# Kernel tuning notes

Measured on AMD Instinct MI355X. Metric: run time of the kernel, lower is better.

The kernel has to match this reference:

```python
import jax, jax.numpy as jnp
import numpy as np

STU_N, EXER_N, K_N, EMB = 20000, 20000, 128, 128
BATCH = 4096

def _pos(w):
    # PosLinear weight transform: 2*relu(-w) + w  (== |w|)
    return 2.0 * jax.nn.relu(-w) + w

def setup_inputs() -> dict:
    key = jax.random.key(0)
    ks = jax.random.split(key, 12)
    xav = lambda k, shape: jax.random.normal(k, shape, jnp.float32) * np.sqrt(2.0 / sum(shape))
    return {
        "stu_id": jax.random.randint(ks[0], (BATCH,), 0, STU_N, jnp.int32),
        "exer_id": jax.random.randint(ks[1], (BATCH,), 0, EXER_N, jnp.int32),
        "kq": jax.random.uniform(ks[2], (BATCH, K_N), jnp.float32),
        "student_q": xav(ks[3], (STU_N, EMB)),
        "exercise_k": xav(ks[4], (EXER_N, EMB)),
        "student_v": xav(ks[5], (STU_N, EMB)),
        "exercise_v": xav(ks[6], (EXER_N, EMB)),
        "knowledge_v": xav(ks[7], (K_N, EMB)),
        "W1": xav(ks[8], (EMB, 2 * EMB)), "b1": jnp.zeros((EMB,), jnp.float32),
        "W2": xav(ks[9], (EMB, 2 * EMB)), "b2": jnp.zeros((EMB,), jnp.float32),
        "W3": xav(ks[10], (1, EMB)), "b3": jnp.zeros((1,), jnp.float32),
    }

def reference(stu_id, exer_id, kq, student_q, exercise_k, student_v, exercise_v,
              knowledge_v, W1, b1, W2, b2, W3, b3):
    stu_q = student_q[stu_id]          # (B, D)
    exer_k = exercise_k[exer_id]       # (B, D)
    stu_v = student_v[stu_id]          # (B, D)
    exer_v = exercise_v[exer_id]       # (B, D)
    B, D = stu_v.shape
    K = knowledge_v.shape[0]

    kn = jnp.broadcast_to(knowledge_v[None, :, :], (B, K, D))
    stu_b = jnp.broadcast_to(stu_v[:, None, :], (B, K, D))
    exer_b = jnp.broadcast_to(exer_v[:, None, :], (B, K, D))

    # PosLinear 1/2 on concat([x, kn]) -> split GEMM avoids materializing concat
    W1p, W2p, W3p = _pos(W1), _pos(W2), _pos(W3)
    pref = jax.nn.sigmoid(jnp.einsum('bkd,ed->bke', jnp.concatenate([stu_b, kn], -1), W1p) + b1)
    diff = jax.nn.sigmoid(jnp.einsum('bkd,ed->bke', jnp.concatenate([exer_b, kn], -1), W2p) + b2)

    disc = jax.nn.sigmoid(stu_q * exer_k)              # (B, D)
    input_x = (pref - diff) * disc[:, None, :]         # (B, K, D)
    o = jax.nn.sigmoid(jnp.einsum('bkd,od->bko', input_x, W3p) + b3)  # (B, K, 1)

    sum_out = jnp.sum(o * kq[:, :, None], axis=1)      # (B, 1)
    count = jnp.sum(kq, axis=1, keepdims=True)         # (B, 1)
    return jnp.squeeze(sum_out / count)                # (B,)
```

## Files before the change

kernel.cpp:

```cpp
#include <hip/hip_runtime.h>

#define D  128
#define KN 128
#define NB 16
#define LOG2E 1.44269504088896340736f

__device__ __forceinline__ float negexp(float v) {
    return __builtin_amdgcn_exp2f(v * -LOG2E);
}
__device__ __forceinline__ float sigf(float x) {
    return __builtin_amdgcn_rcpf(1.0f + negexp(x));
}

__device__ __forceinline__ void emit_row(
    float4* __restrict__ P, int b, int eg,
    const float4& as, const float4& ae,
    const float* __restrict__ stu_q, const float* __restrict__ exer_k,
    const float* __restrict__ kq, const float* __restrict__ W3,
    int sid, int eid)
{
    float4 sq = *(const float4*)(stu_q + sid * D + eg * 4);
    float4 ek = *(const float4*)(exer_k + eid * D + eg * 4);
    float4 kv = *(const float4*)(kq + b * D + eg * 4);
    float4 w3 = *(const float4*)(W3 + eg * 4);
    float4* Pb = P + b * D + eg * 4;
    Pb[0] = make_float4(negexp(as.x), negexp(ae.x), sigf(sq.x * ek.x) * fabsf(w3.x), kv.x);
    Pb[1] = make_float4(negexp(as.y), negexp(ae.y), sigf(sq.y * ek.y) * fabsf(w3.y), kv.y);
    Pb[2] = make_float4(negexp(as.z), negexp(ae.z), sigf(sq.z * ek.z) * fabsf(w3.z), kv.z);
    Pb[3] = make_float4(negexp(as.w), negexp(ae.w), sigf(sq.w * ek.w) * fabsf(w3.w), kv.w);
}

__global__ __launch_bounds__(512) void k1_kernel(
    const int* __restrict__ stu_id, const int* __restrict__ exer_id,
    const float* __restrict__ kq,
    const float* __restrict__ stu_q, const float* __restrict__ exer_k,
    const float* __restrict__ stu_v, const float* __restrict__ exer_v,
    const float* __restrict__ kn,
    const float* __restrict__ W1, const float* __restrict__ b1,
    const float* __restrict__ W2, const float* __restrict__ b2,
    const float* __restrict__ W3,
    float4* __restrict__ P, float* __restrict__ TABGf, int B)
{
    __shared__ float W1T[D][132];
    __shared__ float W2T[D][132];
    __shared__ float SV[NB][D];
    __shared__ float EV[NB][D];
    __shared__ int sids[NB], eids[NB];

    const int tid = threadIdx.x;
    const int b0  = blockIdx.x * NB;

    if (tid < NB) {
        int b = b0 + tid;
        sids[tid] = stu_id[b < B ? b : 0];
        eids[tid] = exer_id[b < B ? b : 0];
    }
    for (int i = tid; i < D * D; i += 512) {
        int e = i >> 7, d = i & (D - 1);
        W1T[d][e] = fabsf(W1[e * (2 * D) + d]);
        W2T[d][e] = fabsf(W2[e * (2 * D) + d]);
    }
    __syncthreads();
    for (int i = tid; i < NB * D; i += 512) {
        int bi = i >> 7, d = i & (D - 1);
        SV[bi][d] = stu_v[sids[bi] * D + d];
        EV[bi][d] = exer_v[eids[bi] * D + d];
    }
    __syncthreads();

    if (tid < 256) {
        const int eg  = tid & 31;
        const int bh  = tid >> 5;
        const int bi0 = 2 * bh, bi1 = 2 * bh + 1;

        float4 as0 = {0, 0, 0, 0}, as1 = as0, ae0 = as0, ae1 = as0;
        #pragma unroll 4
        for (int d = 0; d < D; ++d) {
            float4 w1 = *(const float4*)&W1T[d][eg * 4];
            float4 w2 = *(const float4*)&W2T[d][eg * 4];
            float sv0 = SV[bi0][d], sv1 = SV[bi1][d];
            float ev0 = EV[bi0][d], ev1 = EV[bi1][d];
            as0.x = fmaf(sv0, w1.x, as0.x); as0.y = fmaf(sv0, w1.y, as0.y);
            as0.z = fmaf(sv0, w1.z, as0.z); as0.w = fmaf(sv0, w1.w, as0.w);
            as1.x = fmaf(sv1, w1.x, as1.x); as1.y = fmaf(sv1, w1.y, as1.y);
            as1.z = fmaf(sv1, w1.z, as1.z); as1.w = fmaf(sv1, w1.w, as1.w);
            ae0.x = fmaf(ev0, w2.x, ae0.x); ae0.y = fmaf(ev0, w2.y, ae0.y);
            ae0.z = fmaf(ev0, w2.z, ae0.z); ae0.w = fmaf(ev0, w2.w, ae0.w);
            ae1.x = fmaf(ev1, w2.x, ae1.x); ae1.y = fmaf(ev1, w2.y, ae1.y);
            ae1.z = fmaf(ev1, w2.z, ae1.z); ae1.w = fmaf(ev1, w2.w, ae1.w);
        }
        if (b0 + bi0 < B) emit_row(P, b0 + bi0, eg, as0, ae0, stu_q, exer_k, kq, W3, sids[bi0], eids[bi0]);
        if (b0 + bi1 < B) emit_row(P, b0 + bi1, eg, as1, ae1, stu_q, exer_k, kq, W3, sids[bi1], eids[bi1]);
    } else if (blockIdx.x < 64) {
        const int idx = blockIdx.x * 256 + (tid - 256);
        const int e = idx >> 7, k = idx & (KN - 1);
        const float4* knr = (const float4*)(kn + k * D);
        const float4* w1r = (const float4*)(W1 + e * (2 * D) + D);
        const float4* w2r = (const float4*)(W2 + e * (2 * D) + D);
        float a1 = 0.f, a2 = 0.f;
        #pragma unroll 8
        for (int q = 0; q < D / 4; ++q) {
            float4 kv = knr[q], u = w1r[q], v = w2r[q];
            a1 = fmaf(kv.x, fabsf(u.x), a1); a1 = fmaf(kv.y, fabsf(u.y), a1);
            a1 = fmaf(kv.z, fabsf(u.z), a1); a1 = fmaf(kv.w, fabsf(u.w), a1);
            a2 = fmaf(kv.x, fabsf(v.x), a2); a2 = fmaf(kv.y, fabsf(v.y), a2);
            a2 = fmaf(kv.z, fabsf(v.z), a2); a2 = fmaf(kv.w, fabsf(v.w), a2);
        }
        const int base = e * 256 + (k >> 1) * 4 + (k & 1);
        TABGf[base]     = negexp(a1 + b1[e]);
        TABGf[base + 2] = negexp(a2 + b2[e]);
    }
}

__global__ __launch_bounds__(512) void main_kernel(
    const float4* __restrict__ P, const float4* __restrict__ TABG,
    const float* __restrict__ b3p, float* __restrict__ out, int B)
{
    __shared__ float4 TAB[D * 64];
    __shared__ float4 PW[8][D];

    const int tid = threadIdx.x;
    #pragma unroll
    for (int it = 0; it < 16; ++it) {
        int j = tid + it * 512;
        TAB[j] = TABG[j];
    }
    __syncthreads();

    const int wid = tid >> 6, lane = tid & 63;
    const float b3v = b3p[0];

    for (int ib = wid; ib < 16; ib += 8) {
        const int b = blockIdx.x * 16 + ib;
        if (b >= B) break;
        PW[wid][lane]      = P[b * D + lane];
        PW[wid][lane + 64] = P[b * D + lane + 64];
        float acc0 = 0.f, acc1 = 0.f;
        #pragma unroll 4
        for (int e = 0; e < D; ++e) {
            float4 p = PW[wid][e];
            float4 t = TAB[e * 64 + lane];
            float x0 = fmaf(p.x, t.x, 1.0f);
            float x1 = fmaf(p.x, t.y, 1.0f);
            float y0 = fmaf(p.y, t.z, 1.0f);
            float y1 = fmaf(p.y, t.w, 1.0f);
            float n0 = (y0 - x0) * p.z;
            float n1 = (y1 - x1) * p.z;
            acc0 = fmaf(n0, __builtin_amdgcn_rcpf(x0 * y0), acc0);
            acc1 = fmaf(n1, __builtin_amdgcn_rcpf(x1 * y1), acc1);
        }
        float o0 = sigf(acc0 + b3v);
        float o1 = sigf(acc1 + b3v);
        float kq0 = PW[wid][2 * lane].w;
        float kq1 = PW[wid][2 * lane + 1].w;
        float num = fmaf(o0, kq0, o1 * kq1);
        float den = kq0 + kq1;
        #pragma unroll
        for (int off = 32; off > 0; off >>= 1) {
            num += __shfl_xor(num, off);
            den += __shfl_xor(den, off);
        }
        if (lane == 0) out[b] = num / den;
    }
}

extern "C" void kernel_launch(void* const* d_in, const int* in_sizes, int n_in,
                              void* d_out, int out_size, void* d_ws, size_t ws_size,
                              hipStream_t stream)
{
    const int*   stu_id      = (const int*)  d_in[0];
    const int*   exer_id     = (const int*)  d_in[1];
    const float* kq          = (const float*)d_in[2];
    const float* student_q   = (const float*)d_in[3];
    const float* exercise_k  = (const float*)d_in[4];
    const float* student_v   = (const float*)d_in[5];
    const float* exercise_v  = (const float*)d_in[6];
    const float* knowledge_v = (const float*)d_in[7];
    const float* W1 = (const float*)d_in[8];
    const float* b1 = (const float*)d_in[9];
    const float* W2 = (const float*)d_in[10];
    const float* b2 = (const float*)d_in[11];
    const float* W3 = (const float*)d_in[12];
    const float* b3 = (const float*)d_in[13];
    float* out = (float*)d_out;
    const int B = in_sizes[0];

    float*  TABGf = (float*)d_ws;
    float4* P     = (float4*)((char*)d_ws + (size_t)(D * KN * 2) * sizeof(float));

    int nprep = (B + NB - 1) / NB;
    int grid1 = nprep > 64 ? nprep : 64;
    k1_kernel<<<grid1, 512, 0, stream>>>(
        stu_id, exer_id, kq, student_q, exercise_k, student_v, exercise_v,
        knowledge_v, W1, b1, W2, b2, W3, P, TABGf, B);
    main_kernel<<<(B + 15) / 16, 512, 0, stream>>>(
        P, (const float4*)TABGf, b3, out, B);
}
```

Baseline: 37.17 us.

## Fuse prep and main kernels into one cooperative kernel with grid sync

Merges the two kernels into a single cooperative launch. Each block keeps its per-row precomputed values (exp terms, disc*|W3|) in shared memory instead of writing P to global, then waits on a grid-wide sync for the shared knowledge table before running the main accumulation. Shared memory is reused through a union, and each warp now processes two rows at once. This removes one kernel launch and the P round trip through global memory, at the cost of a grid barrier and one block per CU. The grid is clamped to 256 blocks, which matches the 16-row-per-block work only when B is at most 4096, so larger batches would go unprocessed.

After: 97.09 us. +161.2%, slower.

```diff
diff --git a/kernel.cpp b/kernel.cpp
--- a/kernel.cpp
+++ b/kernel.cpp
@@ -1,4 +1,7 @@
 #include <hip/hip_runtime.h>
+#include <hip/hip_cooperative_groups.h>
+
+namespace cg = cooperative_groups;
 
 #define D  128
 #define KN 128
@@ -12,25 +15,29 @@
     return __builtin_amdgcn_rcpf(1.0f + negexp(x));
 }
 
-__device__ __forceinline__ void emit_row(
-    float4* __restrict__ P, int b, int eg,
-    const float4& as, const float4& ae,
-    const float* __restrict__ stu_q, const float* __restrict__ exer_k,
-    const float* __restrict__ kq, const float* __restrict__ W3,
-    int sid, int eid)
-{
-    float4 sq = *(const float4*)(stu_q + sid * D + eg * 4);
-    float4 ek = *(const float4*)(exer_k + eid * D + eg * 4);
-    float4 kv = *(const float4*)(kq + b * D + eg * 4);
-    float4 w3 = *(const float4*)(W3 + eg * 4);
-    float4* Pb = P + b * D + eg * 4;
-    Pb[0] = make_float4(negexp(as.x), negexp(ae.x), sigf(sq.x * ek.x) * fabsf(w3.x), kv.x);
-    Pb[1] = make_float4(negexp(as.y), negexp(ae.y), sigf(sq.y * ek.y) * fabsf(w3.y), kv.y);
-    Pb[2] = make_float4(negexp(as.z), negexp(ae.z), sigf(sq.z * ek.z) * fabsf(w3.z), kv.z);
-    Pb[3] = make_float4(negexp(as.w), negexp(ae.w), sigf(sq.w * ek.w) * fabsf(w3.w), kv.w);
-}
-
-__global__ __launch_bounds__(512) void k1_kernel(
+struct SharedA {
+    float W1T[D][132];
+    float W2T[D][132];
+    float SV[NB][D];
+    float EV[NB][D];
+};
+struct SharedB {
+    float4 TAB[D * 64];
+    float4 EAp[NB][D / 2];
+    float2 PZp[NB][D / 2];
+};
+union SharedU { SharedA a; SharedB b; };
+
+#define CORE(EA1, EA2, T, PZ, A0, A1) do {                                   \
+    float x0_ = fmaf((EA1), (T).x, 1.0f);                                    \
+    float x1_ = fmaf((EA1), (T).y, 1.0f);                                    \
+    float y0_ = fmaf((EA2), (T).z, 1.0f);                                    \
+    float y1_ = fmaf((EA2), (T).w, 1.0f);                                    \
+    (A0) = fmaf((y0_ - x0_) * (PZ), __builtin_amdgcn_rcpf(x0_ * y0_), (A0)); \
+    (A1) = fmaf((y1_ - x1_) * (PZ), __builtin_amdgcn_rcpf(x1_ * y1_), (A1)); \
+} while (0)
+
+__global__ __launch_bounds__(512, 1) void fused_kernel(
     const int* __restrict__ stu_id, const int* __restrict__ exer_id,
     const float* __restrict__ kq,
     const float* __restrict__ stu_q, const float* __restrict__ exer_k,
@@ -38,48 +45,45 @@
     const float* __restrict__ kn,
     const float* __restrict__ W1, const float* __restrict__ b1,
     const float* __restrict__ W2, const float* __restrict__ b2,
-    const float* __restrict__ W3,
-    float4* __restrict__ P, float* __restrict__ TABGf, int B)
+    const float* __restrict__ W3, const float* __restrict__ b3,
+    float* __restrict__ TABGf, float* __restrict__ out, int B)
 {
-    __shared__ float W1T[D][132];
-    __shared__ float W2T[D][132];
-    __shared__ float SV[NB][D];
-    __shared__ float EV[NB][D];
+    __shared__ SharedU sh;
     __shared__ int sids[NB], eids[NB];
 
-    const int tid = threadIdx.x;
-    const int b0  = blockIdx.x * NB;
+    const int tid   = threadIdx.x;
+    const int b0blk = blockIdx.x * NB;
 
     if (tid < NB) {
-        int b = b0 + tid;
+        int b = b0blk + tid;
         sids[tid] = stu_id[b < B ? b : 0];
         eids[tid] = exer_id[b < B ? b : 0];
     }
     for (int i = tid; i < D * D; i += 512) {
         int e = i >> 7, d = i & (D - 1);
-        W1T[d][e] = fabsf(W1[e * (2 * D) + d]);
-        W2T[d][e] = fabsf(W2[e * (2 * D) + d]);
+        sh.a.W1T[d][e] = fabsf(W1[e * (2 * D) + d]);
+        sh.a.W2T[d][e] = fabsf(W2[e * (2 * D) + d]);
     }
     __syncthreads();
     for (int i = tid; i < NB * D; i += 512) {
         int bi = i >> 7, d = i & (D - 1);
-        SV[bi][d] = stu_v[sids[bi] * D + d];
-        EV[bi][d] = exer_v[eids[bi] * D + d];
-    }
-    __syncthreads();
+        sh.a.SV[bi][d] = stu_v[(size_t)sids[bi] * D + d];
+        sh.a.EV[bi][d] = exer_v[(size_t)eids[bi] * D + d];
+    }
+    __syncthreads();
+
+    const int eg  = tid & 31;
+    const int bh  = (tid >> 5) & 7;
+    const int bi0 = 2 * bh, bi1 = 2 * bh + 1;
+    float4 as0 = {0, 0, 0, 0}, as1 = as0, ae0 = as0, ae1 = as0;
 
     if (tid < 256) {
-        const int eg  = tid & 31;
-        const int bh  = tid >> 5;
-        const int bi0 = 2 * bh, bi1 = 2 * bh + 1;
-
-        float4 as0 = {0, 0, 0, 0}, as1 = as0, ae0 = as0, ae1 = as0;
         #pragma unroll 4
         for (int d = 0; d < D; ++d) {
-            float4 w1 = *(const float4*)&W1T[d][eg * 4];
-            float4 w2 = *(const float4*)&W2T[d][eg * 4];
-            float sv0 = SV[bi0][d], sv1 = SV[bi1][d];
-            float ev0 = EV[bi0][d], ev1 = EV[bi1][d];
+            float4 w1 = *(const float4*)&sh.a.W1T[d][eg * 4];
+            float4 w2 = *(const float4*)&sh.a.W2T[d][eg * 4];
+            float sv0 = sh.a.SV[bi0][d], sv1 = sh.a.SV[bi1][d];
+            float ev0 = sh.a.EV[bi0][d], ev1 = sh.a.EV[bi1][d];
             as0.x = fmaf(sv0, w1.x, as0.x); as0.y = fmaf(sv0, w1.y, as0.y);
             as0.z = fmaf(sv0, w1.z, as0.z); as0.w = fmaf(sv0, w1.w, as0.w);
             as1.x = fmaf(sv1, w1.x, as1.x); as1.y = fmaf(sv1, w1.y, as1.y);
@@ -89,14 +93,12 @@
             ae1.x = fmaf(ev1, w2.x, ae1.x); ae1.y = fmaf(ev1, w2.y, ae1.y);
             ae1.z = fmaf(ev1, w2.z, ae1.z); ae1.w = fmaf(ev1, w2.w, ae1.w);
         }
-        if (b0 + bi0 < B) emit_row(P, b0 + bi0, eg, as0, ae0, stu_q, exer_k, kq, W3, sids[bi0], eids[bi0]);
-        if (b0 + bi1 < B) emit_row(P, b0 + bi1, eg, as1, ae1, stu_q, exer_k, kq, W3, sids[bi1], eids[bi1]);
     } else if (blockIdx.x < 64) {
         const int idx = blockIdx.x * 256 + (tid - 256);
         const int e = idx >> 7, k = idx & (KN - 1);
-        const float4* knr = (const float4*)(kn + k * D);
-        const float4* w1r = (const float4*)(W1 + e * (2 * D) + D);
-        const float4* w2r = (const float4*)(W2 + e * (2 * D) + D);
+        const float4* knr = (const float4*)(kn + (size_t)k * D);
+        const float4* w1r = (const float4*)(W1 + (size_t)e * (2 * D) + D);
+        const float4* w2r = (const float4*)(W2 + (size_t)e * (2 * D) + D);
         float a1 = 0.f, a2 = 0.f;
         #pragma unroll 8
         for (int q = 0; q < D / 4; ++q) {
@@ -110,57 +112,79 @@
         TABGf[base]     = negexp(a1 + b1[e]);
         TABGf[base + 2] = negexp(a2 + b2[e]);
     }
-}
-
-__global__ __launch_bounds__(512) void main_kernel(
-    const float4* __restrict__ P, const float4* __restrict__ TABG,
-    const float* __restrict__ b3p, float* __restrict__ out, int B)
-{
-    __shared__ float4 TAB[D * 64];
-    __shared__ float4 PW[8][D];
-
-    const int tid = threadIdx.x;
+    __syncthreads();
+
+    if (tid < 256) {
+        float4 w3 = *(const float4*)(W3 + eg * 4);
+        float4 w3a = make_float4(fabsf(w3.x), fabsf(w3.y), fabsf(w3.z), fabsf(w3.w));
+        if (b0blk + bi0 < B) {
+            int b = b0blk + bi0;
+            float4 sq = *(const float4*)(stu_q + (size_t)sids[bi0] * D + eg * 4);
+            float4 ek = *(const float4*)(exer_k + (size_t)eids[bi0] * D + eg * 4);
+            sh.b.EAp[bi0][eg*2]   = make_float4(negexp(as0.x), negexp(ae0.x), negexp(as0.y), negexp(ae0.y));
+            sh.b.EAp[bi0][eg*2+1] = make_float4(negexp(as0.z), negexp(ae0.z), negexp(as0.w), negexp(ae0.w));
+            sh.b.PZp[bi0][eg*2]   = make_float2(sigf(sq.x*ek.x)*w3a.x, sigf(sq.y*ek.y)*w3a.y);
+            sh.b.PZp[bi0][eg*2+1] = make_float2(sigf(sq.z*ek.z)*w3a.z, sigf(sq.w*ek.w)*w3a.w);
+            (void)b;
+        }
+        if (b0blk + bi1 < B) {
+            float4 sq = *(const float4*)(stu_q + (size_t)sids[bi1] * D + eg * 4);
+            float4 ek = *(const float4*)(exer_k + (size_t)eids[bi1] * D + eg * 4);
+            sh.b.EAp[bi1][eg*2]   = make_float4(negexp(as1.x), negexp(ae1.x), negexp(as1.y), negexp(ae1.y));
+            sh.b.EAp[bi1][eg*2+1] = make_float4(negexp(as1.z), negexp(ae1.z), negexp(as1.w), negexp(ae1.w));
+            sh.b.PZp[bi1][eg*2]   = make_float2(sigf(sq.x*ek.x)*w3a.x, sigf(sq.y*ek.y)*w3a.y);
+            sh.b.PZp[bi1][eg*2+1] = make_float2(sigf(sq.z*ek.z)*w3a.z, sigf(sq.w*ek.w)*w3a.w);
+        }
+    }
+
+    __threadfence();
+    cg::this_grid().sync();
+
+    const float4* TABG4 = (const float4*)TABGf;
     #pragma unroll
     for (int it = 0; it < 16; ++it) {
         int j = tid + it * 512;
-        TAB[j] = TABG[j];
+        sh.b.TAB[j] = TABG4[j];
     }
     __syncthreads();
 
     const int wid = tid >> 6, lane = tid & 63;
-    const float b3v = b3p[0];
-
-    for (int ib = wid; ib < 16; ib += 8) {
-        const int b = blockIdx.x * 16 + ib;
-        if (b >= B) break;
-        PW[wid][lane]      = P[b * D + lane];
-        PW[wid][lane + 64] = P[b * D + lane + 64];
-        float acc0 = 0.f, acc1 = 0.f;
-        #pragma unroll 4
-        for (int e = 0; e < D; ++e) {
-            float4 p = PW[wid][e];
-            float4 t = TAB[e * 64 + lane];
-            float x0 = fmaf(p.x, t.x, 1.0f);
-            float x1 = fmaf(p.x, t.y, 1.0f);
-            float y0 = fmaf(p.y, t.z, 1.0f);
-            float y1 = fmaf(p.y, t.w, 1.0f);
-            float n0 = (y0 - x0) * p.z;
-            float n1 = (y1 - x1) * p.z;
-            acc0 = fmaf(n0, __builtin_amdgcn_rcpf(x0 * y0), acc0);
-            acc1 = fmaf(n1, __builtin_amdgcn_rcpf(x1 * y1), acc1);
-        }
-        float o0 = sigf(acc0 + b3v);
-        float o1 = sigf(acc1 + b3v);
-        float kq0 = PW[wid][2 * lane].w;
-        float kq1 = PW[wid][2 * lane + 1].w;
-        float num = fmaf(o0, kq0, o1 * kq1);
-        float den = kq0 + kq1;
-        #pragma unroll
-        for (int off = 32; off > 0; off >>= 1) {
-            num += __shfl_xor(num, off);
-            den += __shfl_xor(den, off);
-        }
-        if (lane == 0) out[b] = num / den;
+    const float b3v = b3[0];
+    const int rA = 2 * wid, rB = 2 * wid + 1;
+    const int bA = b0blk + rA, bB = b0blk + rB;
+
+    float acc0a = 0.f, acc1a = 0.f, acc0b = 0.f, acc1b = 0.f;
+    #pragma unroll 2
+    for (int j = 0; j < D / 2; ++j) {
+        float4 t0 = sh.b.TAB[(2 * j) * 64 + lane];
+        float4 t1 = sh.b.TAB[(2 * j + 1) * 64 + lane];
+        float4 eA = sh.b.EAp[rA][j]; float2 zA = sh.b.PZp[rA][j];
+        float4 eB = sh.b.EAp[rB][j]; float2 zB = sh.b.PZp[rB][j];
+        CORE(eA.x, eA.y, t0, zA.x, acc0a, acc1a);
+        CORE(eA.z, eA.w, t1, zA.y, acc0a, acc1a);
+        CORE(eB.x, eB.y, t0, zB.x, acc0b, acc1b);
+        CORE(eB.z, eB.w, t1, zB.y, acc0b, acc1b);
+    }
+
+    float o0a = sigf(acc0a + b3v), o1a = sigf(acc1a + b3v);
+    float o0b = sigf(acc0b + b3v), o1b = sigf(acc1b + b3v);
+    float na = 0.f, da = 0.f, nb = 0.f, db = 0.f;
+    if (bA < B) {
+        float2 kqa = *(const float2*)(kq + (size_t)bA * D + 2 * lane);
+        na = fmaf(o0a, kqa.x, o1a * kqa.y); da = kqa.x + kqa.y;
+    }
+    if (bB < B) {
+        float2 kqb = *(const float2*)(kq + (size_t)bB * D + 2 * lane);
+        nb = fmaf(o0b, kqb.x, o1b * kqb.y); db = kqb.x + kqb.y;
+    }
+    #pragma unroll
+    for (int off = 32; off > 0; off >>= 1) {
+        na += __shfl_xor(na, off); da += __shfl_xor(da, off);
+        nb += __shfl_xor(nb, off); db += __shfl_xor(db, off);
+    }
+    if (lane == 0) {
+        if (bA < B) out[bA] = na / da;
+        if (bB < B) out[bB] = nb / db;
     }
 }
 
@@ -183,16 +207,23 @@
     const float* W3 = (const float*)d_in[12];
     const float* b3 = (const float*)d_in[13];
     float* out = (float*)d_out;
-    const int B = in_sizes[0];
-
-    float*  TABGf = (float*)d_ws;
-    float4* P     = (float4*)((char*)d_ws + (size_t)(D * KN * 2) * sizeof(float));
-
-    int nprep = (B + NB - 1) / NB;
-    int grid1 = nprep > 64 ? nprep : 64;
-    k1_kernel<<<grid1, 512, 0, stream>>>(
-        stu_id, exer_id, kq, student_q, exercise_k, student_v, exercise_v,
-        knowledge_v, W1, b1, W2, b2, W3, P, TABGf, B);
-    main_kernel<<<(B + 15) / 16, 512, 0, stream>>>(
-        P, (const float4*)TABGf, b3, out, B);
-}
+    int B = in_sizes[0];
+
+    float* TABGf = (float*)d_ws;
+
+    int nblk = (B + NB - 1) / NB;
+    if (nblk < 64)  nblk = 64;
+    if (nblk > 256) nblk = 256;
+
+    void* args[] = {
+        (void*)&stu_id, (void*)&exer_id, (void*)&kq,
+        (void*)&student_q, (void*)&exercise_k,
+        (void*)&student_v, (void*)&exercise_v,
+        (void*)&knowledge_v,
+        (void*)&W1, (void*)&b1, (void*)&W2, (void*)&b2,
+        (void*)&W3, (void*)&b3,
+        (void*)&TABGf, (void*)&out, (void*)&B,
+    };
+    hipLaunchCooperativeKernel((void*)fused_kernel, dim3(nblk), dim3(512),
+                               args, 0, stream);
+}
```
